# Optimization experiments

Measured on AMD Instinct MI355X. Metric: run time of the kernel, lower is better.

The kernel has to match this reference:

```python
import jax, jax.numpy as jnp
import numpy as np

EMBED_DIM = 768
NUM_HEADS = 8
HEAD_DIM = EMBED_DIM // NUM_HEADS
SCALE = HEAD_DIM ** -0.5
B = 256
N_TOTAL = 16384


def setup_inputs() -> dict:
    key = jax.random.key(0)
    ks = jax.random.split(key, 10)
    s = 1.0 / np.sqrt(EMBED_DIM)
    inp = {
        "query": jax.random.normal(ks[0], (B, EMBED_DIM), jnp.float32),
        "search": jax.random.normal(ks[1], (N_TOTAL, EMBED_DIM), jnp.float32),
        # q_proj / k_proj: Linear(embed_dim, embed_dim)
        "Wq": jax.random.uniform(ks[2], (EMBED_DIM, EMBED_DIM), jnp.float32, -s, s),
        "bq": jax.random.uniform(ks[3], (EMBED_DIM,), jnp.float32, -s, s),
        "Wk": jax.random.uniform(ks[4], (EMBED_DIM, EMBED_DIM), jnp.float32, -s, s),
        "bk": jax.random.uniform(ks[5], (EMBED_DIM,), jnp.float32, -s, s),
        # score_fusion: Linear(H, H//2) -> GELU -> Linear(H//2, 1)
        "W1": jax.random.uniform(ks[6], (NUM_HEADS // 2, NUM_HEADS), jnp.float32, -1.0 / np.sqrt(NUM_HEADS), 1.0 / np.sqrt(NUM_HEADS)),
        "b1": jax.random.uniform(ks[7], (NUM_HEADS // 2,), jnp.float32, -1.0 / np.sqrt(NUM_HEADS), 1.0 / np.sqrt(NUM_HEADS)),
        "W2": jax.random.uniform(ks[8], (1, NUM_HEADS // 2), jnp.float32, -1.0 / np.sqrt(NUM_HEADS // 2), 1.0 / np.sqrt(NUM_HEADS // 2)),
        "b2": jax.random.uniform(ks[9], (1,), jnp.float32, -1.0 / np.sqrt(NUM_HEADS // 2), 1.0 / np.sqrt(NUM_HEADS // 2)),
    }
    return inp


def reference(query, search, Wq, bq, Wk, bk, W1, b1, W2, b2):
    Bq = query.shape[0]
    Nt = search.shape[0]
    # projections -> (B, H, hd) and (N, H, hd)
    q = (query @ Wq.T + bq).reshape(Bq, NUM_HEADS, HEAD_DIM)
    k = (search @ Wk.T + bk).reshape(Nt, NUM_HEADS, HEAD_DIM)
    # per-head dot products: (B, N, H)
    attn_logits = jnp.einsum('bhd,nhd->bnh', q, k) * SCALE
    # tiny MLP over head axis: H -> H//2 -> 1, exact (erf) GELU as in torch default
    h = jax.nn.gelu(attn_logits @ W1.T + b1, approximate=False)
    scores = h @ W2.T + b2  # (B, N, 1)
    return scores.squeeze(-1)
```

## Files before the change

### kernel.cpp

```cpp
#include <hip/hip_runtime.h>
#include <math.h>

#define SCALE 0.1020620726159658f

typedef __attribute__((ext_vector_type(8))) short shortx8;
typedef __attribute__((ext_vector_type(4))) float floatx4;

__device__ __forceinline__ unsigned short f2bf(float f) {
  union { float f; unsigned int i; } c; c.f = f;
  unsigned int x = c.i;
  x += 0x7fffu + ((x >> 16) & 1u);
  return (unsigned short)(x >> 16);
}
__device__ __forceinline__ float gelu_fast(float x) {
  float x2 = x * x;
  float y = x * (0.7978845608f + 0.0356774081f * x2);
  float e = fminf(y * 2.885390082f, 60.0f);
  float t = exp2f(e);
  return x * t * __builtin_amdgcn_rcpf(t + 1.0f);
}
__device__ __forceinline__ void async_ld16(const unsigned short* g, unsigned short* l) {
  __builtin_amdgcn_global_load_lds(
      (const __attribute__((address_space(1))) unsigned int*)g,
      (__attribute__((address_space(3))) unsigned int*)l, 16, 0, 0);
}
__device__ __forceinline__ void cvt_store8(const float* __restrict__ src,
                                           unsigned short* __restrict__ dst) {
  float4 a = *(const float4*)src;
  float4 b = *(const float4*)(src + 4);
  shortx8 v;
  v[0] = (short)f2bf(a.x); v[1] = (short)f2bf(a.y);
  v[2] = (short)f2bf(a.z); v[3] = (short)f2bf(a.w);
  v[4] = (short)f2bf(b.x); v[5] = (short)f2bf(b.y);
  v[6] = (short)f2bf(b.z); v[7] = (short)f2bf(b.w);
  *(shortx8*)dst = v;
}
__device__ __forceinline__ void mfma_consume(const unsigned short* __restrict__ As,
                                             const unsigned short* __restrict__ Bs,
                                             int wr, int wc, int quad, int l15,
                                             floatx4 (&acc)[4][4]) {
#pragma unroll
  for (int ks = 0; ks < 2; ks++) {
    shortx8 af[4], bfr[4];
#pragma unroll
    for (int mt = 0; mt < 4; mt++) {
      int r = wr * 64 + mt * 16 + l15;
      int ch = (ks * 4 + quad) ^ (r & 7);
      af[mt] = *(const shortx8*)(As + r * 64 + ch * 8);
    }
#pragma unroll
    for (int nt = 0; nt < 4; nt++) {
      int r = wc * 64 + nt * 16 + l15;
      int ch = (ks * 4 + quad) ^ (r & 7);
      bfr[nt] = *(const shortx8*)(Bs + r * 64 + ch * 8);
    }
#pragma unroll
    for (int mt = 0; mt < 4; mt++)
#pragma unroll
      for (int nt = 0; nt < 4; nt++)
        acc[mt][nt] = __builtin_amdgcn_mfma_f32_16x16x32_bf16(
            af[mt], bfr[nt], acc[mt][nt], 0, 0, 0);
  }
}

__global__ __launch_bounds__(256) void k_pre(
    const float* __restrict__ query, const float* __restrict__ Wq,
    const float* __restrict__ bq, const float* __restrict__ W1,
    const float* __restrict__ Wk, const float* __restrict__ search,
    float* __restrict__ qf, unsigned short* __restrict__ QW,
    unsigned short* __restrict__ WkT, unsigned short* __restrict__ sb,
    int use_sb)
{
  __shared__ unsigned short As[64 * 64];
  __shared__ unsigned short Bs[64 * 64];
  __shared__ unsigned short tile[32][33];
  const int bid = blockIdx.x, t = threadIdx.x;
  const int wave = t >> 6, lane = t & 63;
  if (bid < 48) {
    const int by = bid / 12, bx = bid % 12;
    const int m0 = by * 64, n0 = bx * 64;
    const int wr = wave >> 1, wc = wave & 1;
    const int quad = lane >> 4, l15 = lane & 15;
    const int rl = lane >> 3, cL = lane & 7, p = cL ^ rl;
    floatx4 acc[2][2];
#pragma unroll
    for (int i = 0; i < 2; i++)
#pragma unroll
      for (int j = 0; j < 2; j++) acc[i][j] = (floatx4){0.f, 0.f, 0.f, 0.f};
    for (int k0 = 0; k0 < 768; k0 += 64) {
#pragma unroll
      for (int tt = 0; tt < 2; tt++) {
        int r = wave * 16 + tt * 8 + rl;
        cvt_store8(query + (size_t)(m0 + r) * 768 + k0 + cL * 8, As + r * 64 + p * 8);
        cvt_store8(Wq + (size_t)(n0 + r) * 768 + k0 + cL * 8, Bs + r * 64 + p * 8);
      }
      __syncthreads();
#pragma unroll
      for (int ks = 0; ks < 2; ks++) {
        shortx8 af[2], bfr[2];
#pragma unroll
        for (int mt = 0; mt < 2; mt++) {
          int r = wr * 32 + mt * 16 + l15;
          int ch = (ks * 4 + quad) ^ (r & 7);
          af[mt] = *(const shortx8*)(As + r * 64 + ch * 8);
        }
#pragma unroll
        for (int nt = 0; nt < 2; nt++) {
          int r = wc * 32 + nt * 16 + l15;
          int ch = (ks * 4 + quad) ^ (r & 7);
          bfr[nt] = *(const shortx8*)(Bs + r * 64 + ch * 8);
        }
#pragma unroll
        for (int mt = 0; mt < 2; mt++)
#pragma unroll
          for (int nt = 0; nt < 2; nt++)
            acc[mt][nt] = __builtin_amdgcn_mfma_f32_16x16x32_bf16(
                af[mt], bfr[nt], acc[mt][nt], 0, 0, 0);
      }
      __syncthreads();
    }
    const int lrow = quad * 4;
#pragma unroll
    for (int mt = 0; mt < 2; mt++)
#pragma unroll
      for (int nt = 0; nt < 2; nt++) {
        int gm = m0 + wr * 32 + mt * 16 + lrow;
        int gn = n0 + wc * 32 + nt * 16 + l15;
        float bz = bq[gn];
        int h = gn / 96;
        float w1h0 = W1[h], w1h1 = W1[8 + h], w1h2 = W1[16 + h], w1h3 = W1[24 + h];
#pragma unroll
        for (int r = 0; r < 4; r++) {
          float qv = acc[mt][nt][r] + bz;
          qf[(size_t)(gm + r) * 768 + gn] = qv;
          size_t base = (size_t)((gm + r) * 4) * 768 + gn;
          QW[base]           = f2bf(SCALE * w1h0 * qv);
          QW[base + 768]     = f2bf(SCALE * w1h1 * qv);
          QW[base + 2 * 768] = f2bf(SCALE * w1h2 * qv);
          QW[base + 3 * 768] = f2bf(SCALE * w1h3 * qv);
        }
      }
  } else if (bid < 624) {
    const int tb = bid - 48, bx = tb % 24, by = tb / 24;
    const int tx = t & 31, ty = t >> 5;
#pragma unroll
    for (int i = 0; i < 4; i++)
      tile[ty + i * 8][tx] = f2bf(Wk[(size_t)(by * 32 + ty + i * 8) * 768 + bx * 32 + tx]);
    __syncthreads();
#pragma unroll
    for (int i = 0; i < 4; i++)
      WkT[(size_t)(bx * 32 + ty + i * 8) * 768 + by * 32 + tx] = tile[tx][ty + i * 8];
  } else {
    const int fid = bid - 624;
    const int x = fid & 7, idx = fid >> 3;
    const size_t base = ((size_t)(2048 * x + 16 * idx)) * 768;
#pragma unroll
    for (int j = 0; j < 6; j++) {
      size_t i = base + j * 2048 + t * 8;
      cvt_store8(search + i, sb + i);
    }
  }
}

__global__ __launch_bounds__(256) void k_mid(
    const unsigned short* __restrict__ QW, const unsigned short* __restrict__ WkT,
    unsigned short* __restrict__ QQ,
    const float* __restrict__ qf, const float* __restrict__ W1,
    const float* __restrict__ b1, const float* __restrict__ bk,
    float* __restrict__ cp)
{
  __shared__ unsigned short As[64 * 64];
  __shared__ unsigned short Bs[64 * 64];
  const int bid = blockIdx.x, t = threadIdx.x;
  const int wave = t >> 6, lane = t & 63;
  if (bid < 192) {
    const int by = bid / 12, bx = bid % 12;
    const int m0 = by * 64, n0 = bx * 64;
    const int wr = wave >> 1, wc = wave & 1;
    const int quad = lane >> 4, l15 = lane & 15;
    const int rl = lane >> 3, cl = (lane & 7) ^ rl;
    floatx4 acc[2][2];
#pragma unroll
    for (int i = 0; i < 2; i++)
#pragma unroll
      for (int j = 0; j < 2; j++) acc[i][j] = (floatx4){0.f, 0.f, 0.f, 0.f};
    for (int k0 = 0; k0 < 768; k0 += 64) {
#pragma unroll
      for (int tt = 0; tt < 2; tt++) {
        int rr = wave * 16 + tt * 8;
        async_ld16(QW + (size_t)(m0 + rr + rl) * 768 + k0 + cl * 8, As + rr * 64);
        async_ld16(WkT + (size_t)(n0 + rr + rl) * 768 + k0 + cl * 8, Bs + rr * 64);
      }
      __syncthreads();
#pragma unroll
      for (int ks = 0; ks < 2; ks++) {
        shortx8 af[2], bfr[2];
#pragma unroll
        for (int mt = 0; mt < 2; mt++) {
          int r = wr * 32 + mt * 16 + l15;
          int ch = (ks * 4 + quad) ^ (r & 7);
          af[mt] = *(const shortx8*)(As + r * 64 + ch * 8);
        }
#pragma unroll
        for (int nt = 0; nt < 2; nt++) {
          int r = wc * 32 + nt * 16 + l15;
          int ch = (ks * 4 + quad) ^ (r & 7);
          bfr[nt] = *(const shortx8*)(Bs + r * 64 + ch * 8);
        }
#pragma unroll
        for (int mt = 0; mt < 2; mt++)
#pragma unroll
          for (int nt = 0; nt < 2; nt++)
            acc[mt][nt] = __builtin_amdgcn_mfma_f32_16x16x32_bf16(
                af[mt], bfr[nt], acc[mt][nt], 0, 0, 0);
      }
      __syncthreads();
    }
    const int lrow = quad * 4;
#pragma unroll
    for (int mt = 0; mt < 2; mt++)
#pragma unroll
      for (int nt = 0; nt < 2; nt++) {
        int gm = m0 + wr * 32 + mt * 16 + lrow;
        int gn = n0 + wc * 32 + nt * 16 + l15;
#pragma unroll
        for (int r = 0; r < 4; r++)
          QQ[(size_t)(gm + r) * 768 + gn] = f2bf(acc[mt][nt][r]);
      }
  } else {
    const int bstart = (bid - 192) * 64;
    for (int b = bstart + wave; b < bstart + 64; b += 4) {
      const float* qrow = qf + (size_t)b * 768;
      int e0 = lane * 12;
      float s = 0.f;
#pragma unroll
      for (int i = 0; i < 12; i++) s += qrow[e0 + i] * bk[e0 + i];
      s += __shfl_xor(s, 1); s += __shfl_xor(s, 2); s += __shfl_xor(s, 4);
      float v = __shfl(s, (lane & 7) * 8);
      float w = W1[((lane >> 3) & 3) * 8 + (lane & 7)] * v;
      w += __shfl_xor(w, 1); w += __shfl_xor(w, 2); w += __shfl_xor(w, 4);
      if (lane < 32 && (lane & 7) == 0) {
        int j = lane >> 3;
        cp[b * 4 + j] = b1[j] + SCALE * w;
      }
    }
  }
}

__global__ __launch_bounds__(256) void k_main(
    const unsigned short* __restrict__ QQ, const void* __restrict__ Bv,
    float* __restrict__ out, const float* __restrict__ cp,
    const float* __restrict__ W2, const float* __restrict__ b2, int use_sb)
{
  __shared__ unsigned short As[128 * 64];
  __shared__ unsigned short Bs[128 * 64];
  const int bid = blockIdx.x;
  const int n_tile = (bid & 7) * 16 + ((bid >> 3) & 15);
  const int m_tile = bid >> 7;
  const int m0 = m_tile * 128, n0 = n_tile * 128;
  const int t = threadIdx.x, wave = t >> 6, lane = t & 63;
  const int wr = wave >> 1, wc = wave & 1;
  const int quad = lane >> 4, l15 = lane & 15;
  floatx4 acc[4][4];
#pragma unroll
  for (int i = 0; i < 4; i++)
#pragma unroll
    for (int j = 0; j < 4; j++) acc[i][j] = (floatx4){0.f, 0.f, 0.f, 0.f};
  const int rl = lane >> 3, cl = (lane & 7) ^ rl, cL = lane & 7, p = cL ^ rl;
  for (int k0 = 0; k0 < 768; k0 += 64) {
#pragma unroll
    for (int tt = 0; tt < 4; tt++) {
      int rr = wave * 32 + tt * 8;
      async_ld16(QQ + (size_t)(m0 + rr + rl) * 768 + k0 + cl * 8, As + rr * 64);
    }
    if (use_sb) {
      const unsigned short* B16 = (const unsigned short*)Bv;
#pragma unroll
      for (int tt = 0; tt < 4; tt++) {
        int rr = wave * 32 + tt * 8;
        async_ld16(B16 + (size_t)(n0 + rr + rl) * 768 + k0 + cl * 8, Bs + rr * 64);
      }
    } else {
      const float* Bf = (const float*)Bv;
#pragma unroll
      for (int tt = 0; tt < 4; tt++) {
        int r = wave * 32 + tt * 8 + rl;
        cvt_store8(Bf + (size_t)(n0 + r) * 768 + k0 + cL * 8, Bs + r * 64 + p * 8);
      }
    }
    __syncthreads();
    mfma_consume(As, Bs, wr, wc, quad, l15, acc);
    __syncthreads();
  }
  const float w2v0 = W2[0], w2v1 = W2[1], w2v2 = W2[2], w2v3 = W2[3];
  const float b2v = b2[0];
  const int lrow = quad * 4;
#pragma unroll
  for (int mt = 0; mt < 4; mt++) {
    int gm = m0 + wr * 64 + mt * 16 + lrow;
    float cpv0 = cp[gm], cpv1 = cp[gm + 1], cpv2 = cp[gm + 2], cpv3 = cp[gm + 3];
#pragma unroll
    for (int nt = 0; nt < 4; nt++) {
      int gn = n0 + wc * 64 + nt * 16 + l15;
      floatx4 v = acc[mt][nt];
      float s = b2v;
      s += w2v0 * gelu_fast(v[0] + cpv0);
      s += w2v1 * gelu_fast(v[1] + cpv1);
      s += w2v2 * gelu_fast(v[2] + cpv2);
      s += w2v3 * gelu_fast(v[3] + cpv3);
      out[(size_t)(gm >> 2) * 16384 + gn] = s;
    }
  }
}

extern "C" void kernel_launch(void* const* d_in, const int* in_sizes, int n_in,
                              void* d_out, int out_size, void* d_ws, size_t ws_size,
                              hipStream_t stream) {
  const float* query  = (const float*)d_in[0];
  const float* search = (const float*)d_in[1];
  const float* Wq     = (const float*)d_in[2];
  const float* bq     = (const float*)d_in[3];
  const float* Wk     = (const float*)d_in[4];
  const float* bk     = (const float*)d_in[5];
  const float* W1     = (const float*)d_in[6];
  const float* b1     = (const float*)d_in[7];
  const float* W2     = (const float*)d_in[8];
  const float* b2     = (const float*)d_in[9];
  float* out = (float*)d_out;

  char* ws = (char*)d_ws;
  float*          cp  = (float*)ws;
  float*          qf  = (float*)(ws + 4352);
  unsigned short* WkT = (unsigned short*)(ws + 790784);
  unsigned short* QW  = (unsigned short*)(ws + 1970432);
  unsigned short* QQ  = (unsigned short*)(ws + 3543296);
  unsigned short* sb  = (unsigned short*)(ws + 5116160);
  int use_sb = (ws_size >= 30281984u) ? 1 : 0;

  k_pre<<<use_sb ? 1648 : 624, 256, 0, stream>>>(query, Wq, bq, W1, Wk, search,
                                                 qf, QW, WkT, sb, use_sb);
  k_mid<<<196, 256, 0, stream>>>(QW, WkT, QQ, qf, W1, b1, bk, cp);
  k_main<<<1024, 256, 0, stream>>>(QQ, use_sb ? (const void*)sb : (const void*)search,
                                   out, cp, W2, b2, use_sb);
}
```

Before: 168.9 us.

## Double-buffer the B tile in LDS and read A fragments straight from global

Moves the B (search) tile into a two-stage LDS buffer so the load for step k+1 is issued before the MFMAs for step k run. This leaves one barrier per iteration instead of two. The A (query projection) fragments are no longer staged in LDS; each wave loads them directly from global memory into registers. The aim is to hide global-load latency behind compute and cut LDS traffic and barrier stalls. The cost is more registers and redundant global reads of A, since the two waves in each row group load the same A rows.

```diff
diff --git a/kernel.cpp b/kernel.cpp
--- a/kernel.cpp
+++ b/kernel.cpp
@@ -252,8 +252,7 @@
     float* __restrict__ out, const float* __restrict__ cp,
     const float* __restrict__ W2, const float* __restrict__ b2, int use_sb)
 {
-  __shared__ unsigned short As[128 * 64];
-  __shared__ unsigned short Bs[128 * 64];
+  __shared__ unsigned short Bs[2][128 * 64];
   const int bid = blockIdx.x;
   const int n_tile = (bid & 7) * 16 + ((bid >> 3) & 15);
   const int m_tile = bid >> 7;
@@ -267,31 +266,71 @@
 #pragma unroll
     for (int j = 0; j < 4; j++) acc[i][j] = (floatx4){0.f, 0.f, 0.f, 0.f};
   const int rl = lane >> 3, cl = (lane & 7) ^ rl, cL = lane & 7, p = cL ^ rl;
-  for (int k0 = 0; k0 < 768; k0 += 64) {
+  const unsigned short* B16 = (const unsigned short*)Bv;
+  const float* Bf = (const float*)Bv;
+
+  if (use_sb) {
 #pragma unroll
     for (int tt = 0; tt < 4; tt++) {
       int rr = wave * 32 + tt * 8;
-      async_ld16(QQ + (size_t)(m0 + rr + rl) * 768 + k0 + cl * 8, As + rr * 64);
-    }
-    if (use_sb) {
-      const unsigned short* B16 = (const unsigned short*)Bv;
-#pragma unroll
-      for (int tt = 0; tt < 4; tt++) {
-        int rr = wave * 32 + tt * 8;
-        async_ld16(B16 + (size_t)(n0 + rr + rl) * 768 + k0 + cl * 8, Bs + rr * 64);
-      }
-    } else {
-      const float* Bf = (const float*)Bv;
-#pragma unroll
-      for (int tt = 0; tt < 4; tt++) {
-        int r = wave * 32 + tt * 8 + rl;
-        cvt_store8(Bf + (size_t)(n0 + r) * 768 + k0 + cL * 8, Bs + r * 64 + p * 8);
-      }
-    }
+      async_ld16(B16 + (size_t)(n0 + rr + rl) * 768 + cl * 8, Bs[0] + rr * 64);
+    }
+  } else {
+#pragma unroll
+    for (int tt = 0; tt < 4; tt++) {
+      int r = wave * 32 + tt * 8 + rl;
+      cvt_store8(Bf + (size_t)(n0 + r) * 768 + cL * 8, Bs[0] + r * 64 + p * 8);
+    }
+  }
+
+  for (int i = 0; i < 12; i++) {
+    const int k0 = i * 64;
     __syncthreads();
-    mfma_consume(As, Bs, wr, wc, quad, l15, acc);
-    __syncthreads();
-  }
+    if (i < 11) {
+      const int k1 = k0 + 64;
+      if (use_sb) {
+#pragma unroll
+        for (int tt = 0; tt < 4; tt++) {
+          int rr = wave * 32 + tt * 8;
+          async_ld16(B16 + (size_t)(n0 + rr + rl) * 768 + k1 + cl * 8,
+                     Bs[(i + 1) & 1] + rr * 64);
+        }
+      } else {
+#pragma unroll
+        for (int tt = 0; tt < 4; tt++) {
+          int r = wave * 32 + tt * 8 + rl;
+          cvt_store8(Bf + (size_t)(n0 + r) * 768 + k1 + cL * 8,
+                     Bs[(i + 1) & 1] + r * 64 + p * 8);
+        }
+      }
+    }
+    shortx8 af[2][4];
+#pragma unroll
+    for (int ks = 0; ks < 2; ks++)
+#pragma unroll
+      for (int mt = 0; mt < 4; mt++) {
+        int r = m0 + wr * 64 + mt * 16 + l15;
+        af[ks][mt] = *(const shortx8*)(QQ + (size_t)r * 768 + k0 + ks * 32 + quad * 8);
+      }
+    const unsigned short* bbuf = Bs[i & 1];
+#pragma unroll
+    for (int ks = 0; ks < 2; ks++) {
+      shortx8 bfr[4];
+#pragma unroll
+      for (int nt = 0; nt < 4; nt++) {
+        int r = wc * 64 + nt * 16 + l15;
+        int ch = (ks * 4 + quad) ^ (r & 7);
+        bfr[nt] = *(const shortx8*)(bbuf + r * 64 + ch * 8);
+      }
+#pragma unroll
+      for (int mt = 0; mt < 4; mt++)
+#pragma unroll
+        for (int nt = 0; nt < 4; nt++)
+          acc[mt][nt] = __builtin_amdgcn_mfma_f32_16x16x32_bf16(
+              af[ks][mt], bfr[nt], acc[mt][nt], 0, 0, 0);
+    }
+  }
+
   const float w2v0 = W2[0], w2v1 = W2[1], w2v2 = W2[2], w2v3 = W2[3];
   const float b2v = b2[0];
   const int lrow = quad * 4;
```

Result: slower. 194.5 us (+15.2%).
